# Kernel optimization log

Hardware: AMD Instinct MI355X
Metric: run time of the kernel (lower is better)

The kernel has to match this reference:

```python
import jax, jax.numpy as jnp
import numpy as np

HEADS, DIM_HEAD, DIM = 12, 64, 768
H = W = 32
N = H * W
B = 4


def _ln(x, g, b, eps=1e-5):
    mu = x.mean(-1, keepdims=True)
    var = ((x - mu) ** 2).mean(-1, keepdims=True)
    return (x - mu) / jnp.sqrt(var + eps) * g + b


def _get_epipolar(k, src_c2w, target_c2w, h=H, w=W):
    # Faithful port of Epipolar_Attention.get_epipolar, without the (hw*hw,3) repeat
    # materialization (uses broadcasting for the pairwise cross product instead).
    b = k.shape[0]
    Wf = h * 16.0 / 9.0
    k = k.astype(jnp.float32)
    k = k.at[:, 0, :].multiply(Wf).at[:, 1, :].multiply(float(h))
    k = k.at[:, 0, 2].set(h / 2.0).at[:, 1, 2].set(h / 2.0)
    ii, jj = jnp.meshgrid(jnp.arange(h), jnp.arange(w), indexing='ij')
    # after the torch column swap: (col, row, 1)
    coords = jnp.stack([jj.ravel(), ii.ravel(), jnp.ones(h * w, jnp.int32)], axis=1).astype(jnp.float32)  # [hw,3]
    k3 = k[:, :3, :3]
    src_r, src_t = src_c2w[:, :3, :3].astype(jnp.float32), src_c2w[:, :3, 3].astype(jnp.float32)
    tgt_r, tgt_t = target_c2w[:, :3, :3].astype(jnp.float32), target_c2w[:, :3, 3].astype(jnp.float32)
    tgt_rinv = jnp.linalg.inv(tgt_r)
    fx, fy = k3[:, 0, 0][:, None], k3[:, 1, 1][:, None]
    cx, cy = k3[:, 0, 2][:, None], k3[:, 1, 2][:, None]
    nc = jnp.stack([(coords[None, :, 0] - cx) / fx,
                    (coords[None, :, 1] - cy) / fy,
                    jnp.broadcast_to(coords[None, :, 2], (b, h * w))], axis=-1)  # [b,hw,3]
    p3w = jnp.einsum('bij,bnj->bni', src_r, nc) + src_t[:, None]
    p2 = jnp.einsum('bij,bnj->bni', tgt_rinv, p3w) - tgt_t[:, None]  # target_w2c_t = -target_c2w_t
    pij_un = jnp.einsum('bij,bnj->bni', k3, p2)                      # [b,hw,3]
    pij = pij_un / (pij_un[..., -1:] + 1e-6)
    o2 = jnp.einsum('bij,bj->bi', tgt_rinv, src_t) - tgt_t           # origin projected
    oij = jnp.einsum('bij,bj->bi', k3, o2)
    oij = oij / oij[..., -1:]
    oi_to_pi = pij - oij[:, None]                # [b,hw,3]
    oi_to_coord = coords[None] - oij[:, None]    # [b,hw,3]
    cr = jnp.cross(oi_to_pi[:, :, None, :], oi_to_coord[:, None, :, :])  # [b,hw,hw,3]
    area = jnp.sqrt((cr * cr).sum(-1))
    vlen = jnp.sqrt((oi_to_pi * oi_to_pi).sum(-1))[:, :, None]
    dist = area / vlen
    dw = 1.0 - jax.nn.sigmoid(50.0 * (dist - 0.5))
    row_max = dw.max(-1, keepdims=True)
    return jnp.where(row_max < 0.5, 1.0, dw)     # rows with max<0.5 are set to all-ones


def setup_inputs():
    key = jax.random.key(0)
    ks = jax.random.split(key, 16)
    s = 0.02
    x = jax.random.normal(ks[0], (B, N, DIM), jnp.float32)
    src_encode = jax.random.normal(ks[1], (B, N, DIM), jnp.float32)
    intrinsic = (jnp.zeros((B, 4, 4), jnp.float32)
                 .at[:, 0, 0].set(1.0).at[:, 1, 1].set(1.0)
                 .at[:, 0, 2].set(0.5).at[:, 1, 2].set(0.5)
                 .at[:, 2, 2].set(1.0).at[:, 3, 3].set(1.0))
    R = jnp.eye(3, dtype=jnp.float32) + 0.1 * jax.random.normal(ks[2], (2, B, 3, 3), jnp.float32)
    t = 0.5 * jax.random.normal(ks[3], (2, B, 3), jnp.float32)
    c2w = (jnp.zeros((2, B, 4, 4), jnp.float32)
           .at[:, :, :3, :3].set(R).at[:, :, :3, 3].set(t).at[:, :, 3, 3].set(1.0))
    hd = HEADS * DIM_HEAD
    w_ = lambda k_, shp: s * jax.random.normal(k_, shp, jnp.float32)
    return dict(
        x=x, src_encode=src_encode, intrinsic=intrinsic, c2w=c2w,
        lnq_g=jnp.ones(DIM), lnq_b=jnp.zeros(DIM), Wq=w_(ks[4], (DIM, hd)), bq=jnp.zeros(hd),
        lnk_g=jnp.ones(DIM), lnk_b=jnp.zeros(DIM), Wk=w_(ks[5], (DIM, hd)), bk=jnp.zeros(hd),
        lnv_g=jnp.ones(DIM), lnv_b=jnp.zeros(DIM), Wv=w_(ks[6], (DIM, hd)), bv=jnp.zeros(hd),
        Wp=w_(ks[7], (hd, DIM)), bp=jnp.zeros(DIM),
        pre_g=jnp.ones(DIM), pre_b=jnp.zeros(DIM),
        W1=w_(ks[8], (DIM, 2 * DIM)), b1=jnp.zeros(2 * DIM),
        W2=w_(ks[9], (2 * DIM, DIM)), b2=jnp.zeros(DIM),
        post_g=jnp.ones(DIM), post_b=jnp.zeros(DIM))


def reference(x, src_encode, intrinsic, c2w, lnq_g, lnq_b, Wq, bq, lnk_g, lnk_b, Wk, bk,
              lnv_g, lnv_b, Wv, bv, Wp, bp, pre_g, pre_b, W1, b1, W2, b2, post_g, post_b):
    b, n, _ = x.shape
    scale = DIM_HEAD ** -0.5
    split = lambda t_: t_.reshape(b, n, HEADS, DIM_HEAD).transpose(0, 2, 1, 3)  # [b,m,n,d]
    q = split(_ln(x, lnq_g, lnq_b) @ Wq + bq)
    k = split(_ln(src_encode, lnk_g, lnk_b) @ Wk + bk)
    v = split(_ln(src_encode, lnv_g, lnv_b) @ Wv + bv)
    scores = scale * jnp.einsum('bmqd,bmkd->bmqk', q, k)
    e1 = _get_epipolar(intrinsic, c2w[1], c2w[0])                    # do_epipolar
    e2 = jnp.swapaxes(_get_epipolar(intrinsic, c2w[0], c2w[1]), 1, 2)  # bidirectional (transposed)
    wmap = e1 * e2                                                   # [b,n,n], shared across heads
    att = jax.nn.softmax(scores * wmap[:, None], axis=-1)
    a = jnp.einsum('bmqk,bmkd->bmqd', att, v).transpose(0, 2, 1, 3).reshape(b, n, HEADS * DIM_HEAD)
    z = _ln(a @ Wp + bp, pre_g, pre_b)
    z = z + (jax.nn.gelu(z @ W1 + b1, approximate=False) @ W2 + b2)  # torch nn.GELU = exact erf
    z = _ln(z, post_g, post_b)
    wm_full = jnp.broadcast_to(wmap[:, None], (b, HEADS, n, n)).reshape(b * HEADS, n, n)
    return z, wm_full
```

## Files before the change

### kernel.cpp

```cpp
#include <hip/hip_runtime.h>
#include <hip/hip_bf16.h>

typedef unsigned short u16;
typedef __attribute__((ext_vector_type(4))) unsigned short u16x4;
typedef __attribute__((ext_vector_type(8))) unsigned short u16x8;
typedef __attribute__((ext_vector_type(8))) short s16x8;
typedef __attribute__((ext_vector_type(4))) float f32x4;

#define HEADS 12
#define NSEQ 1024
#define DIMM 768
#define DHEAD 64

__device__ __forceinline__ float b2f(u16 h) {
  union { unsigned u; float f; } v; v.u = ((unsigned)h) << 16; return v.f;
}
__device__ __forceinline__ u16 f2b(float f) {
  union { float f; unsigned u; } v; v.f = f;
  unsigned r = v.u + 0x7fffu + ((v.u >> 16) & 1u);
  return (u16)(r >> 16);
}
__device__ __forceinline__ void gl_lds16(const u16* g, u16* l) {
  __builtin_amdgcn_global_load_lds(
      (const __attribute__((address_space(1))) void*)g,
      (__attribute__((address_space(3))) void*)l, 16, 0, 0);
}

template<bool GELU, bool RESID, bool VTOUT>
__device__ __forceinline__ void gemm64(
    const u16* __restrict__ A, const u16* __restrict__ BT,
    const float* __restrict__ bias, const u16* __restrict__ resid,
    const float* __restrict__ rg, const float* __restrict__ rb,
    u16* __restrict__ C, int K, int lda, int ldb, int ldc,
    int m0, int n0, u16* As, u16* Bs, u16* __restrict__ vt)
{
  const int tid = threadIdx.x;
  const int lane = tid & 63;
  const int wv = tid >> 6;
  const int wm0 = (wv >> 1) * 32;
  const int wn0 = (wv & 1) * 32;
  const int l15 = lane & 15;
  const int quad = lane >> 4;
  const int srow = wv * 8 + (lane >> 3);
  const int schunk = lane & 7;
  const int scol = (schunk ^ (srow & 7)) * 8;

  f32x4 acc[2][2];
  #pragma unroll
  for (int i = 0; i < 2; ++i)
    #pragma unroll
    for (int j = 0; j < 2; ++j)
      acc[i][j] = {0.f, 0.f, 0.f, 0.f};

  const u16* Ab = A + (long)(m0 + srow) * lda + scol;
  const u16* Bb = BT + (long)(n0 + srow) * ldb + scol;

  auto issue = [&](int buf, int kk) {
    #pragma unroll
    for (int s = 0; s < 2; ++s) {
      gl_lds16(Ab + kk + (long)s * 32 * lda, As + buf * 4096 + s * 2048 + wv * 512);
      gl_lds16(Bb + kk + (long)s * 32 * ldb, Bs + buf * 4096 + s * 2048 + wv * 512);
    }
  };

  const int NK = K >> 6;
  issue(0, 0);
  issue(1, 64);

  int cur = 0;
  for (int i = 0; i < NK; ++i) {
    if (i + 1 < NK) asm volatile("s_waitcnt vmcnt(4)" ::: "memory");
    else            asm volatile("s_waitcnt vmcnt(0)" ::: "memory");
    __builtin_amdgcn_s_barrier();
    __builtin_amdgcn_sched_barrier(0);
    if (i + 2 < NK) {
      int nb = cur + 2; if (nb >= 3) nb -= 3;
      issue(nb, (i + 2) * 64);
    }
    const u16* Ac = As + cur * 4096;
    const u16* Bc = Bs + cur * 4096;
    #pragma unroll
    for (int kk = 0; kk < 2; ++kk) {
      s16x8 af[2], bfr[2];
      #pragma unroll
      for (int i2 = 0; i2 < 2; ++i2)
        af[i2] = *(const s16x8*)&Ac[(wm0 + i2 * 16 + l15) * 64 +
                                    (((kk * 4 + quad) ^ (l15 & 7)) * 8)];
      #pragma unroll
      for (int j = 0; j < 2; ++j)
        bfr[j] = *(const s16x8*)&Bc[(wn0 + j * 16 + l15) * 64 +
                                    (((kk * 4 + quad) ^ (l15 & 7)) * 8)];
      #pragma unroll
      for (int i2 = 0; i2 < 2; ++i2)
        #pragma unroll
        for (int j = 0; j < 2; ++j)
          acc[i2][j] = __builtin_amdgcn_mfma_f32_16x16x32_bf16(af[i2], bfr[j], acc[i2][j], 0, 0, 0);
    }
    ++cur; if (cur == 3) cur = 0;
  }

  if (VTOUT) {
    __syncthreads();
    u16* shp = As;
    const int b = m0 >> 10;
    const int nloc = m0 & 1023;
    const int fb0 = n0 - 768;
    #pragma unroll
    for (int j = 0; j < 2; ++j) {
      const float bvv = bias[n0 + wn0 + j * 16 + l15];
      #pragma unroll
      for (int i = 0; i < 2; ++i)
        #pragma unroll
        for (int v = 0; v < 4; ++v)
          shp[(wm0 + i * 16 + quad * 4 + v) * 72 + (wn0 + j * 16 + l15)] =
              f2b(acc[i][j][v] + bvv);
    }
    __syncthreads();
    const int f = tid >> 2;
    const int nb = (tid & 3) * 16;
    u16x8 o0, o1;
    #pragma unroll
    for (int nn = 0; nn < 8; ++nn) {
      o0[nn] = shp[(nb + nn) * 72 + f];
      o1[nn] = shp[(nb + 8 + nn) * 72 + f];
    }
    u16* dst = vt + ((long)(b * 768 + fb0 + f)) * NSEQ + nloc + nb;
    *(u16x8*)&dst[0] = o0;
    *(u16x8*)&dst[8] = o1;
    return;
  }

  #pragma unroll
  for (int i = 0; i < 2; ++i)
    #pragma unroll
    for (int j = 0; j < 2; ++j) {
      const int col = n0 + wn0 + j * 16 + l15;
      const float bvv = bias[col];
      #pragma unroll
      for (int v = 0; v < 4; ++v) {
        const int row = m0 + wm0 + i * 16 + quad * 4 + v;
        float val = acc[i][j][v] + bvv;
        if (GELU) val = 0.5f * val * (1.0f + erff(val * 0.70710678118654752440f));
        if (RESID) val += b2f(resid[(long)row * ldc + col]) * rg[col] + rb[col];
        C[(long)row * ldc + col] = f2b(val);
      }
    }
}

template<bool GELU, bool RESID>
__global__ __launch_bounds__(256)
void gemm_one(const u16* __restrict__ A, const u16* __restrict__ BT,
              const float* __restrict__ bias, const u16* __restrict__ resid,
              const float* __restrict__ rg, const float* __restrict__ rb,
              u16* __restrict__ C, int K, int lda, int ldb, int ldc)
{
  __shared__ u16 As[12288], Bs[12288];
  const int total = gridDim.x * gridDim.y;
  const int fid = blockIdx.y * gridDim.x + blockIdx.x;
  const int swz = (fid & 7) * (total >> 3) + (fid >> 3);
  const int x = swz & 63;
  const int y = swz >> 6;
  gemm64<GELU, RESID, false>(A, BT, bias, resid, rg, rb, C, K, lda, ldb, ldc,
                             x * 64, y * 64, As, Bs, nullptr);
}

__device__ __forceinline__ float dwval(f32x4 U, float ox, float oy, float oz, int m)
{
  const float cx = (float)(m & 31) - ox;
  const float cy = (float)(m >> 5) - oy;
  const float cz = 1.0f - oz;
  const float crx = U.y * cz - U.z * cy;
  const float cry = U.z * cx - U.x * cz;
  const float crz = U.x * cy - U.y * cx;
  const float area = sqrtf(crx * crx + cry * cry + crz * crz);
  const float dist = area / U.w;
  const float t = 50.0f * (dist - 0.5f);
  return 1.0f - 1.0f / (1.0f + __expf(-t));
}

#define PREP_T0 13824
#define PREP_T1 14016
#define PREP_T2 22208
#define PREP_T3 30400

__global__ __launch_bounds__(256)
void prep2(const float* w0, const float* w1, const float* w2,
           const float* w3, const float* w4, const float* w5,
           const float* gq, const float* gk, const float* gv, const float* gp,
           u16* d0, u16* d12, u16* d3, u16* d4, u16* d5,
           const float* bq, const float* bk, const float* bv, const float* b1,
           const float* lnqb, const float* lnkb, const float* lnvb, const float* preb,
           float* obq, float* obkv, float* ob1,
           const float* intr, const float* c2w,
           float* u4, float* oijb, float* flags,
           const float* nx, const float* nsrc, u16* onx, u16* onsrc)
{
  const int bid = blockIdx.x;
  const int tid = threadIdx.x;

  if (bid < PREP_T0) {
    __shared__ u16 t[32][36];
    const int z = bid / 2304;
    const int rem = bid - z * 2304;
    const int bx = rem % 48, by = rem / 48;
    const float* src; const float* g; u16* dst; int R, C; float sc = 1.0f;
    switch (z) {
      case 0: src = w0; g = gq; dst = d0;  R = 768;  C = 768;  sc = 0.125f; break;
      case 1: src = w1; g = gk; dst = d12; R = 768;  C = 768;  break;
      case 2: src = w2; g = gv; dst = d12 + 768 * 768; R = 768; C = 768; break;
      case 3: src = w3; g = nullptr; dst = d3; R = 768;  C = 768;  break;
      case 4: src = w4; g = gp; dst = d4; R = 768;  C = 1536; break;
      default: src = w5; g = nullptr; dst = d5; R = 1536; C = 768; break;
    }
    const int c0 = bx * 32;
    const int r0 = by * 32;
    if (c0 >= C || r0 >= R) return;
    const int i = tid >> 3;
    const int j4 = (tid & 7) * 4;
    const float rs = (g ? g[r0 + i] : 1.0f) * sc;
    #pragma unroll
    for (int jj = 0; jj < 4; ++jj)
      t[i][j4 + jj] = f2b(src[(long)(r0 + i) * C + c0 + j4 + jj] * rs);
    __syncthreads();
    u16x4 ov;
    #pragma unroll
    for (int jj = 0; jj < 4; ++jj) ov[jj] = t[j4 + jj][i];
    *(u16x4*)&dst[(long)(c0 + i) * R + r0 + j4] = ov;
    return;
  }

  if (bid < PREP_T1) {
    __shared__ float red[8][32];
    const int idx = bid - PREP_T0;
    const int y = idx / 48;
    const int bx = idx % 48;
    const float* W; const float* bln; const float* bw; float* out;
    int C; float sc = 1.0f;
    switch (y) {
      case 0: W = w0; bln = lnqb; bw = bq; out = obq;        C = 768;  sc = 0.125f; break;
      case 1: W = w1; bln = lnkb; bw = bk; out = obkv;       C = 768;  break;
      case 2: W = w2; bln = lnvb; bw = bv; out = obkv + 768; C = 768;  break;
      default: W = w4; bln = preb; bw = b1; out = ob1;       C = 1536; break;
    }
    const int c0 = bx * 32;
    if (c0 >= C) return;
    const int cl = tid & 31;
    const int rg = tid >> 5;
    const int c = c0 + cl;
    float s = 0.f;
    for (int r = rg * 96; r < rg * 96 + 96; ++r)
      s += bln[r] * W[(long)r * C + c];
    red[rg][cl] = s;
    __syncthreads();
    if (rg == 0) {
      float tot = bw[c];
      #pragma unroll
      for (int k = 0; k < 8; ++k) tot += red[k][cl];
      out[c] = tot * sc;
    }
    return;
  }

  if (bid < PREP_T2) {
    __shared__ float S[40];
    __shared__ float redf[8];
    const int rowid = bid - PREP_T1;
    const int db = rowid >> 10;
    const int n = rowid & 1023;
    const int d = db >> 2, b = db & 3;
    if (tid == 0) {
      const int sidx = (d == 0) ? 1 : 0;
      const int tidx = 1 - sidx;
      float k3[9], sr[9], st[3], tr[9], tt[3];
      const float Wf = 32.0f * 16.0f / 9.0f;
      for (int j = 0; j < 3; ++j) {
        k3[j]     = intr[(b * 4 + 0) * 4 + j] * Wf;
        k3[3 + j] = intr[(b * 4 + 1) * 4 + j] * 32.0f;
        k3[6 + j] = intr[(b * 4 + 2) * 4 + j];
      }
      k3[2] = 16.0f; k3[5] = 16.0f;
      for (int i = 0; i < 3; ++i) {
        for (int j = 0; j < 3; ++j) {
          sr[i * 3 + j] = c2w[((sidx * 4 + b) * 4 + i) * 4 + j];
          tr[i * 3 + j] = c2w[((tidx * 4 + b) * 4 + i) * 4 + j];
        }
        st[i] = c2w[((sidx * 4 + b) * 4 + i) * 4 + 3];
        tt[i] = c2w[((tidx * 4 + b) * 4 + i) * 4 + 3];
      }
      double a = tr[0], bb_ = tr[1], c = tr[2];
      double dd2 = tr[3], e = tr[4], f = tr[5];
      double g2 = tr[6], h2 = tr[7], i2 = tr[8];
      double det = a * (e * i2 - f * h2) - bb_ * (dd2 * i2 - f * g2) + c * (dd2 * h2 - e * g2);
      double inv[9] = {
        (e * i2 - f * h2), (c * h2 - bb_ * i2), (bb_ * f - c * e),
        (f * g2 - dd2 * i2), (a * i2 - c * g2), (c * dd2 - a * f),
        (dd2 * h2 - e * g2), (bb_ * g2 - a * h2), (a * e - bb_ * dd2)
      };
      float tri[9];
      for (int t2 = 0; t2 < 9; ++t2) tri[t2] = (float)(inv[t2] / det);
      float o2[3], oij[3];
      for (int i3 = 0; i3 < 3; ++i3)
        o2[i3] = tri[i3 * 3] * st[0] + tri[i3 * 3 + 1] * st[1] + tri[i3 * 3 + 2] * st[2] - tt[i3];
      for (int i3 = 0; i3 < 3; ++i3)
        oij[i3] = k3[i3 * 3] * o2[0] + k3[i3 * 3 + 1] * o2[1] + k3[i3 * 3 + 2] * o2[2];
      const float ozf = oij[2];
      oij[0] = oij[0] / ozf; oij[1] = oij[1] / ozf; oij[2] = ozf / ozf;
      if (n == 0) {
        oijb[db * 4 + 0] = oij[0]; oijb[db * 4 + 1] = oij[1];
        oijb[db * 4 + 2] = oij[2]; oijb[db * 4 + 3] = 0.f;
      }
      const float ncx = ((float)(n & 31) - k3[2]) / k3[0];
      const float ncy = ((float)(n >> 5) - k3[5]) / k3[4];
      const float p0 = sr[0] * ncx + sr[1] * ncy + sr[2] + st[0];
      const float p1 = sr[3] * ncx + sr[4] * ncy + sr[5] + st[1];
      const float p2 = sr[6] * ncx + sr[7] * ncy + sr[8] + st[2];
      const float q0 = tri[0] * p0 + tri[1] * p1 + tri[2] * p2 - tt[0];
      const float q1 = tri[3] * p0 + tri[4] * p1 + tri[5] * p2 - tt[1];
      const float q2 = tri[6] * p0 + tri[7] * p1 + tri[8] * p2 - tt[2];
      const float ww0 = k3[0] * q0 + k3[1] * q1 + k3[2] * q2;
      const float ww1 = k3[3] * q0 + k3[4] * q1 + k3[5] * q2;
      const float ww2 = k3[6] * q0 + k3[7] * q1 + k3[8] * q2;
      const float pz = ww2 + 1e-6f;
      const float ux = ww0 / pz - oij[0];
      const float uy = ww1 / pz - oij[1];
      const float uz = ww2 / pz - oij[2];
      const float vlen = sqrtf(ux * ux + uy * uy + uz * uz);
      f32x4 uo = {ux, uy, uz, vlen};
      *(f32x4*)&u4[(long)rowid * 4] = uo;
      S[33] = oij[0]; S[34] = oij[1]; S[35] = oij[2];
      S[36] = ux; S[37] = uy; S[38] = uz; S[39] = vlen;
    }
    __syncthreads();
    const f32x4 U = {S[36], S[37], S[38], S[39]};
    const float ox = S[33], oy = S[34], oz = S[35];
    float mx = -1e30f;
    #pragma unroll
    for (int i = 0; i < 4; ++i)
      mx = fmaxf(mx, dwval(U, ox, oy, oz, tid + i * 256));
    #pragma unroll
    for (int off = 32; off; off >>= 1) mx = fmaxf(mx, __shfl_down(mx, off));
    const int lane = tid & 63, wid = tid >> 6;
    if (!lane) redf[wid] = mx;
    __syncthreads();
    if (!tid) {
      const float m4 = fmaxf(fmaxf(redf[0], redf[1]), fmaxf(redf[2], redf[3]));
      flags[rowid] = (m4 < 0.5f) ? 1.0f : 0.0f;
    }
    return;
  }

  {
    __shared__ float s1[8], s2[8];
    const int r = bid - PREP_T2;
    const float* p = ((r < 4096) ? nx : nsrc) + (long)(r & 4095) * DIMM;
    u16* o = ((r < 4096) ? onx : onsrc) + (long)(r & 4095) * DIMM;
    float v0 = p[tid], v1 = p[tid + 256], v2 = p[tid + 512];
    float s = v0 + v1 + v2;
    #pragma unroll
    for (int off = 32; off; off >>= 1) s += __shfl_down(s, off);
    const int lane = tid & 63, wid = tid >> 6;
    if (!lane) s1[wid] = s;
    __syncthreads();
    if (!tid) s1[4] = s1[0] + s1[1] + s1[2] + s1[3];
    __syncthreads();
    const float mu = s1[4] / 768.0f;
    float d0 = v0 - mu, d1 = v1 - mu, d2 = v2 - mu;
    float sq = d0 * d0 + d1 * d1 + d2 * d2;
    #pragma unroll
    for (int off = 32; off; off >>= 1) sq += __shfl_down(sq, off);
    if (!lane) s2[wid] = sq;
    __syncthreads();
    if (!tid) s2[4] = s2[0] + s2[1] + s2[2] + s2[3];
    __syncthreads();
    const float rstd = 1.0f / sqrtf(s2[4] / 768.0f + 1e-5f);
    o[tid]       = f2b(d0 * rstd);
    o[tid + 256] = f2b(d1 * rstd);
    o[tid + 512] = f2b(d2 * rstd);
  }
}

__global__ __launch_bounds__(256)
void stageB(const u16* __restrict__ nx, const u16* __restrict__ ns,
            const u16* __restrict__ qT, const u16* __restrict__ kvT,
            const float* __restrict__ bqf, const float* __restrict__ bkvf,
            u16* __restrict__ qb, u16* __restrict__ kvb, u16* __restrict__ vT,
            const float* __restrict__ u4, const float* __restrict__ oijb,
            const float* __restrict__ flags,
            u16* __restrict__ wm2, float* __restrict__ wm_full)
{
  __shared__ __align__(16) u16 sh[24576];
  const int bid = blockIdx.x;
  const int tid = threadIdx.x;

  if (bid < 2304) {
    u16* As = sh;
    u16* Bs = sh + 12288;
    const int swz = (bid & 7) * 288 + (bid >> 3);
    const int z = swz / 768;
    const int idx = swz - z * 768;
    const int x = idx & 63;
    const int y = idx >> 6;
    if (z == 0)
      gemm64<false, false, false>(nx, qT, bqf, nullptr, nullptr, nullptr, qb,
                                  768, 768, 768, 768,
                                  x * 64, y * 64, As, Bs, nullptr);
    else if (z == 1)
      gemm64<false, false, false>(ns, kvT, bkvf, nullptr, nullptr, nullptr, kvb,
                                  768, 768, 768, 1536,
                                  x * 64, y * 64, As, Bs, nullptr);
    else
      gemm64<false, false, true>(ns, kvT, bkvf, nullptr, nullptr, nullptr, nullptr,
                                 768, 768, 768, 1536,
                                 x * 64, 768 + y * 64, As, Bs, vT);
    return;
  }

  const int id = bid - 2304;
  const int qx = id & 31;
  const int ky = (id >> 5) & 31;
  const int b = id >> 10;
  const int q0 = qx * 32;
  const int k0 = ky * 32;
  const int i = tid >> 3;
  const int j4 = (tid & 7) * 4;

  f32x4* U2s = (f32x4*)sh;
  float* f2s = (float*)(sh + 256);
  float* f1s = (float*)(sh + 320);
  if (tid < 32) {
    U2s[tid] = *(const f32x4*)&u4[((long)(4 + b) * 1024 + k0 + tid) * 4];
    f2s[tid] = flags[(4 + b) * 1024 + k0 + tid];
    f1s[tid] = flags[b * 1024 + q0 + tid];
  }
  __syncthreads();

  const int q = q0 + i;
  const f32x4 U1 = *(const f32x4*)&u4[((long)b * 1024 + q) * 4];
  const float o1x = oijb[b * 4 + 0], o1y = oijb[b * 4 + 1], o1z = oijb[b * 4 + 2];
  const float o2x = oijb[(4 + b) * 4 + 0], o2y = oijb[(4 + b) * 4 + 1], o2z = oijb[(4 + b) * 4 + 2];
  const bool fl1 = f1s[i] > 0.5f;

  const int Q = q >> 6;
  const int qr = q & 63;
  const int wv2 = qr >> 4, qd = (qr >> 2) & 3, v2 = qr & 3;
  const int kt = (k0 + j4) >> 6;
  u16* w2base = wm2 + ((((long)b * 16 + Q) * 16 + kt) * 256) * 16;

  f32x4 wf;
  #pragma unroll
  for (int jj = 0; jj < 4; ++jj) {
    const int k = k0 + j4 + jj;
    const float e1 = fl1 ? 1.0f : dwval(U1, o1x, o1y, o1z, k);
    const float e2 = (f2s[j4 + jj] > 0.5f) ? 1.0f : dwval(U2s[j4 + jj], o2x, o2y, o2z, q);
    const float w = e1 * e2;
    wf[jj] = w;
    const int kc = k & 63;
    const int j2 = kc >> 4, l2 = kc & 15;
    const int ftid = wv2 * 64 + qd * 16 + l2;
    w2base[ftid * 16 + j2 * 4 + v2] = f2b(w);
  }
  #pragma unroll
  for (int h = 0; h < HEADS; ++h)
    *(f32x4*)&wm_full[((long)(b * HEADS + h) * 1024 + q0 + i) * 1024 + k0 + j4] = wf;
}

__global__ __launch_bounds__(256, 3)
void fattn(const u16* __restrict__ qb, const u16* __restrict__ kvb,
           const u16* __restrict__ vT, const u16* __restrict__ wm2,
           u16* __restrict__ outA)
{
  __shared__ u16 Qs[2 * 64 * 32];
  __shared__ u16 Ks[2][2 * 64 * 32];
  __shared__ u16 Vs[2][2 * 64 * 32];
  __shared__ u16 Ps[64][72];

  const int fid = blockIdx.x;
  const int swz = (fid & 7) * 96 + (fid >> 3);
  const int b = swz / 192;
  const int r = swz - b * 192;
  const int x = r / 12;
  const int h = r - x * 12;
  const int bh = b * HEADS + h;
  const int q0 = x * 64;
  const int tid = threadIdx.x;
  const int lane = tid & 63;
  const int wv = tid >> 6;
  const int l15 = lane & 15;
  const int quad = lane >> 4;
  const int srow = lane >> 2;
  const int sscol = ((lane & 3) ^ ((lane >> 3) & 3)) * 8;
  const int rch = (quad ^ ((l15 >> 1) & 3)) * 8;

  const u16* Qg = qb + ((long)b * NSEQ + q0) * DIMM + h * DHEAD;
  const u16* Kg = kvb + (long)b * NSEQ * 1536 + h * DHEAD;
  const u16* Vg = vT + (long)bh * DHEAD * NSEQ;
  const u16* W2 = wm2 + ((((long)b * 16 + x) * 16) * 256) * 16;

  #pragma unroll
  for (int h2 = 0; h2 < 2; ++h2) {
    gl_lds16(Qg + (long)(wv * 16 + srow) * DIMM + h2 * 32 + sscol,
             Qs + (h2 * 64 + wv * 16) * 32);
    gl_lds16(Kg + (long)(wv * 16 + srow) * 1536 + h2 * 32 + sscol,
             Ks[0] + (h2 * 64 + wv * 16) * 32);
    gl_lds16(Vg + (long)(wv * 16 + srow) * NSEQ + h2 * 32 + sscol,
             Vs[0] + (h2 * 64 + wv * 16) * 32);
  }

  f32x4 Sacc[4], Oacc[4];
  float mrow[4], lrow[4];
  #pragma unroll
  for (int j = 0; j < 4; ++j) {
    Oacc[j] = {0.f, 0.f, 0.f, 0.f};
    mrow[j] = -3.0e38f;
    lrow[j] = 0.f;
  }
  s16x8 qf[2];

  int cur = 0;
  for (int kt = 0; kt < 16; ++kt) {
    __syncthreads();
    if (kt < 15) {
      const int nxt = cur ^ 1;
      #pragma unroll
      for (int h2 = 0; h2 < 2; ++h2) {
        gl_lds16(Kg + (long)((kt + 1) * 64 + wv * 16 + srow) * 1536 + h2 * 32 + sscol,
                 Ks[nxt] + (h2 * 64 + wv * 16) * 32);
        gl_lds16(Vg + (long)(wv * 16 + srow) * NSEQ + (kt + 1) * 64 + h2 * 32 + sscol,
                 Vs[nxt] + (h2 * 64 + wv * 16) * 32);
      }
    }

    if (kt == 0) {
      qf[0] = *(const s16x8*)&Qs[(0 * 64 + wv * 16 + l15) * 32 + rch];
      qf[1] = *(const s16x8*)&Qs[(1 * 64 + wv * 16 + l15) * 32 + rch];
    }

    const u16x8 wa = *(const u16x8*)&W2[((long)kt * 256 + tid) * 16];
    const u16x8 wb = *(const u16x8*)&W2[((long)kt * 256 + tid) * 16 + 8];
    float wr[4][4];
    #pragma unroll
    for (int v = 0; v < 4; ++v) {
      wr[0][v] = b2f(wa[v]);
      wr[1][v] = b2f(wa[4 + v]);
      wr[2][v] = b2f(wb[v]);
      wr[3][v] = b2f(wb[4 + v]);
    }

    #pragma unroll
    for (int j = 0; j < 4; ++j) Sacc[j] = {0.f, 0.f, 0.f, 0.f};
    #pragma unroll
    for (int j = 0; j < 4; ++j)
      #pragma unroll
      for (int h2 = 0; h2 < 2; ++h2) {
        s16x8 kf = *(const s16x8*)&Ks[cur][(h2 * 64 + j * 16 + l15) * 32 + rch];
        Sacc[j] = __builtin_amdgcn_mfma_f32_16x16x32_bf16(qf[h2], kf, Sacc[j], 0, 0, 0);
      }

    #pragma unroll
    for (int j = 0; j < 4; ++j)
      #pragma unroll
      for (int v = 0; v < 4; ++v)
        Sacc[j][v] *= wr[j][v];
    #pragma unroll
    for (int v = 0; v < 4; ++v) {
      float tm = fmaxf(fmaxf(Sacc[0][v], Sacc[1][v]), fmaxf(Sacc[2][v], Sacc[3][v]));
      tm = fmaxf(tm, __shfl_xor(tm, 1));
      tm = fmaxf(tm, __shfl_xor(tm, 2));
      tm = fmaxf(tm, __shfl_xor(tm, 4));
      tm = fmaxf(tm, __shfl_xor(tm, 8));
      const float mnew = fmaxf(mrow[v], tm);
      const float al = __expf(mrow[v] - mnew);
      float rs = 0.f;
      #pragma unroll
      for (int j = 0; j < 4; ++j) {
        const float e = __expf(Sacc[j][v] - mnew);
        Sacc[j][v] = e;
        rs += e;
      }
      rs += __shfl_xor(rs, 1);
      rs += __shfl_xor(rs, 2);
      rs += __shfl_xor(rs, 4);
      rs += __shfl_xor(rs, 8);
      lrow[v] = lrow[v] * al + rs;
      mrow[v] = mnew;
      #pragma unroll
      for (int jn = 0; jn < 4; ++jn) Oacc[jn][v] *= al;
    }
    #pragma unroll
    for (int j = 0; j < 4; ++j)
      #pragma unroll
      for (int v = 0; v < 4; ++v)
        Ps[wv * 16 + quad * 4 + v][j * 16 + l15] = f2b(Sacc[j][v]);

    #pragma unroll
    for (int h2 = 0; h2 < 2; ++h2) {
      s16x8 af = *(const s16x8*)&Ps[wv * 16 + l15][h2 * 32 + quad * 8];
      #pragma unroll
      for (int jn = 0; jn < 4; ++jn) {
        s16x8 vf = *(const s16x8*)&Vs[cur][(h2 * 64 + jn * 16 + l15) * 32 + rch];
        Oacc[jn] = __builtin_amdgcn_mfma_f32_16x16x32_bf16(af, vf, Oacc[jn], 0, 0, 0);
      }
    }
    cur ^= 1;
  }

  #pragma unroll
  for (int v = 0; v < 4; ++v) {
    const int row = q0 + wv * 16 + quad * 4 + v;
    const float inv = 1.0f / lrow[v];
    #pragma unroll
    for (int jn = 0; jn < 4; ++jn)
      outA[((long)(b * NSEQ + row)) * DIMM + h * DHEAD + jn * 16 + l15] =
          f2b(Oacc[jn][v] * inv);
  }
}

__global__ __launch_bounds__(256)
void norm_k(const u16* __restrict__ in, u16* __restrict__ out)
{
  const long base = (long)blockIdx.x * DIMM;
  const int tid = threadIdx.x;
  __shared__ float s1[8], s2[8];
  const u16* p = in + base;
  float v0 = b2f(p[tid]), v1 = b2f(p[tid + 256]), v2 = b2f(p[tid + 512]);
  float s = v0 + v1 + v2;
  #pragma unroll
  for (int off = 32; off; off >>= 1) s += __shfl_down(s, off);
  const int lane = tid & 63, wid = tid >> 6;
  if (!lane) s1[wid] = s;
  __syncthreads();
  if (!tid) s1[4] = s1[0] + s1[1] + s1[2] + s1[3];
  __syncthreads();
  const float mu = s1[4] / 768.0f;
  float d0 = v0 - mu, d1 = v1 - mu, d2 = v2 - mu;
  float sq = d0 * d0 + d1 * d1 + d2 * d2;
  #pragma unroll
  for (int off = 32; off; off >>= 1) sq += __shfl_down(sq, off);
  if (!lane) s2[wid] = sq;
  __syncthreads();
  if (!tid) s2[4] = s2[0] + s2[1] + s2[2] + s2[3];
  __syncthreads();
  const float rstd = 1.0f / sqrtf(s2[4] / 768.0f + 1e-5f);
  u16* o = out + base;
  o[tid]       = f2b(d0 * rstd);
  o[tid + 256] = f2b(d1 * rstd);
  o[tid + 512] = f2b(d2 * rstd);
}

__global__ __launch_bounds__(256)
void ln_final(const u16* __restrict__ in, const float* __restrict__ g,
              const float* __restrict__ bb, float* __restrict__ out)
{
  const long base = (long)blockIdx.x * DIMM;
  const int tid = threadIdx.x;
  __shared__ float s1[8], s2[8];
  const u16* p = in + base;
  float v0 = b2f(p[tid]), v1 = b2f(p[tid + 256]), v2 = b2f(p[tid + 512]);
  float s = v0 + v1 + v2;
  #pragma unroll
  for (int off = 32; off; off >>= 1) s += __shfl_down(s, off);
  const int lane = tid & 63, wid = tid >> 6;
  if (!lane) s1[wid] = s;
  __syncthreads();
  if (!tid) s1[4] = s1[0] + s1[1] + s1[2] + s1[3];
  __syncthreads();
  const float mu = s1[4] / 768.0f;
  float d0 = v0 - mu, d1 = v1 - mu, d2 = v2 - mu;
  float sq = d0 * d0 + d1 * d1 + d2 * d2;
  #pragma unroll
  for (int off = 32; off; off >>= 1) sq += __shfl_down(sq, off);
  if (!lane) s2[wid] = sq;
  __syncthreads();
  if (!tid) s2[4] = s2[0] + s2[1] + s2[2] + s2[3];
  __syncthreads();
  const float rstd = 1.0f / sqrtf(s2[4] / 768.0f + 1e-5f);
  float* o = out + base;
  o[tid]       = d0 * rstd * g[tid]       + bb[tid];
  o[tid + 256] = d1 * rstd * g[tid + 256] + bb[tid + 256];
  o[tid + 512] = d2 * rstd * g[tid + 512] + bb[tid + 512];
}

extern "C" void kernel_launch(void* const* d_in, const int* in_sizes, int n_in,
                              void* d_out, int out_size, void* d_ws, size_t ws_size,
                              hipStream_t stream)
{
  (void)in_sizes; (void)n_in; (void)out_size; (void)ws_size;
  const float* x     = (const float*)d_in[0];
  const float* src   = (const float*)d_in[1];
  const float* intr  = (const float*)d_in[2];
  const float* c2w   = (const float*)d_in[3];
  const float* lnq_g = (const float*)d_in[4];
  const float* lnq_b = (const float*)d_in[5];
  const float* Wq    = (const float*)d_in[6];
  const float* bq    = (const float*)d_in[7];
  const float* lnk_g = (const float*)d_in[8];
  const float* lnk_b = (const float*)d_in[9];
  const float* Wk    = (const float*)d_in[10];
  const float* bk    = (const float*)d_in[11];
  const float* lnv_g = (const float*)d_in[12];
  const float* lnv_b = (const float*)d_in[13];
  const float* Wv    = (const float*)d_in[14];
  const float* bv    = (const float*)d_in[15];
  const float* Wp    = (const float*)d_in[16];
  const float* bp    = (const float*)d_in[17];
  const float* pre_g = (const float*)d_in[18];
  const float* pre_b = (const float*)d_in[19];
  const float* W1    = (const float*)d_in[20];
  const float* b1    = (const float*)d_in[21];
  const float* W2    = (const float*)d_in[22];
  const float* b2    = (const float*)d_in[23];
  const float* post_g= (const float*)d_in[24];
  const float* post_b= (const float*)d_in[25];

  char* ws = (char*)d_ws;
  size_t off = 0;
  auto alloc = [&](size_t bytes) -> char* {
    char* p = ws + off;
    off = (off + bytes + 255) & ~(size_t)255;
    return p;
  };
  const size_t SEQD = (size_t)4096 * 768 * 2;

  u16* WqT  = (u16*)alloc(768 * 768 * 2);
  u16* WkvT = (u16*)alloc((size_t)1536 * 768 * 2);
  u16* WpT  = (u16*)alloc(768 * 768 * 2);
  u16* W1T  = (u16*)alloc(768 * 1536 * 2);
  u16* W2T  = (u16*)alloc(1536 * 768 * 2);
  float* bqf  = (float*)alloc(768 * 4);
  float* bkvf = (float*)alloc(1536 * 4);
  float* b1f  = (float*)alloc(1536 * 4);
  char* pool = alloc(6 * SEQD);
  float* u4   = (float*)alloc(8 * 1024 * 4 * 4);
  float* oijb = (float*)alloc(8 * 4 * 4);
  u16* wm2b   = (u16*)alloc((size_t)4 * 1024 * 1024 * 2);
  float* flagb = (float*)alloc(8 * 1024 * 4);

  u16* S0 = (u16*)pool;
  u16* S1 = (u16*)(pool + SEQD);
  u16* S2 = (u16*)(pool + 2 * SEQD);
  u16* S3 = (u16*)(pool + 3 * SEQD);
  u16* S5 = (u16*)(pool + 5 * SEQD);

  float* out_z  = (float*)d_out;
  float* out_wm = (float*)d_out + (size_t)4 * 1024 * 768;

  prep2<<<PREP_T3, 256, 0, stream>>>(
      Wq, Wk, Wv, Wp, W1, W2, lnq_g, lnk_g, lnv_g, pre_g,
      WqT, WkvT, WpT, W1T, W2T,
      bq, bk, bv, b1, lnq_b, lnk_b, lnv_b, pre_b,
      bqf, bkvf, b1f,
      intr, c2w, u4, oijb, flagb,
      x, src, S0, S1);

  stageB<<<6400, 256, 0, stream>>>(
      S0, S1, WqT, WkvT, bqf, bkvf, S2, S3, S5,
      u4, oijb, flagb, wm2b, out_wm);

  fattn<<<768, 256, 0, stream>>>(S2, S3, S5, wm2b, S0);

  gemm_one<false, false><<<dim3(64, 12), 256, 0, stream>>>(
      S0, WpT, bp, nullptr, nullptr, nullptr, S1, 768, 768, 768, 768);

  norm_k<<<4096, 256, 0, stream>>>(S1, S2);

  gemm_one<true, false><<<dim3(64, 24), 256, 0, stream>>>(
      S2, W1T, b1f, nullptr, nullptr, nullptr, S3, 768, 768, 768, 1536);

  gemm_one<false, true><<<dim3(64, 12), 256, 0, stream>>>(
      S3, W2T, b2, S2, pre_g, pre_b, S5, 1536, 1536, 1536, 768);

  ln_final<<<4096, 256, 0, stream>>>(S5, post_g, post_b, out_z);
}
```

Baseline: 467.1 us.

## Enlarge GEMM tiles to 128x128 with double buffering and nontemporal weight-map stores

Every GEMM now uses 128x128 block tiles: each wave computes a 64x64 sub-tile with a 4x4 MFMA accumulator array, and a 2-stage LDS buffer replaces the 3-stage ring. Grid sizes and the stageB block split are updated to match, and the V-transpose epilogue is done in two 64-row passes. The aim is more operand reuse and fewer global loads per FLOP. In exchange there are far fewer blocks (192-576 per GEMM on a 256-CU part), more registers per wave, and a shallower prefetch pipeline. The large wm_full broadcast writes also become nontemporal stores to reduce cache pollution.

```diff
diff --git a/kernel.cpp b/kernel.cpp
--- a/kernel.cpp
+++ b/kernel.cpp
@@ -27,7 +27,7 @@
 }
 
 template<bool GELU, bool RESID, bool VTOUT>
-__device__ __forceinline__ void gemm64(
+__device__ __forceinline__ void gemm128(
     const u16* __restrict__ A, const u16* __restrict__ BT,
     const float* __restrict__ bias, const u16* __restrict__ resid,
     const float* __restrict__ rg, const float* __restrict__ rb,
@@ -37,19 +37,18 @@
   const int tid = threadIdx.x;
   const int lane = tid & 63;
   const int wv = tid >> 6;
-  const int wm0 = (wv >> 1) * 32;
-  const int wn0 = (wv & 1) * 32;
+  const int wm0 = (wv >> 1) * 64;
+  const int wn0 = (wv & 1) * 64;
   const int l15 = lane & 15;
   const int quad = lane >> 4;
   const int srow = wv * 8 + (lane >> 3);
-  const int schunk = lane & 7;
-  const int scol = (schunk ^ (srow & 7)) * 8;
-
-  f32x4 acc[2][2];
-  #pragma unroll
-  for (int i = 0; i < 2; ++i)
-    #pragma unroll
-    for (int j = 0; j < 2; ++j)
+  const int scol = ((lane & 7) ^ (lane >> 3)) * 8;
+
+  f32x4 acc[4][4];
+  #pragma unroll
+  for (int i = 0; i < 4; ++i)
+    #pragma unroll
+    for (int j = 0; j < 4; ++j)
       acc[i][j] = {0.f, 0.f, 0.f, 0.f};
 
   const u16* Ab = A + (long)(m0 + srow) * lda + scol;
@@ -57,83 +56,85 @@
 
   auto issue = [&](int buf, int kk) {
     #pragma unroll
-    for (int s = 0; s < 2; ++s) {
-      gl_lds16(Ab + kk + (long)s * 32 * lda, As + buf * 4096 + s * 2048 + wv * 512);
-      gl_lds16(Bb + kk + (long)s * 32 * ldb, Bs + buf * 4096 + s * 2048 + wv * 512);
+    for (int s = 0; s < 4; ++s) {
+      gl_lds16(Ab + kk + (long)s * 32 * lda, As + buf * 8192 + s * 2048 + wv * 512);
+      gl_lds16(Bb + kk + (long)s * 32 * ldb, Bs + buf * 8192 + s * 2048 + wv * 512);
     }
   };
 
   const int NK = K >> 6;
   issue(0, 0);
-  issue(1, 64);
 
   int cur = 0;
   for (int i = 0; i < NK; ++i) {
-    if (i + 1 < NK) asm volatile("s_waitcnt vmcnt(4)" ::: "memory");
-    else            asm volatile("s_waitcnt vmcnt(0)" ::: "memory");
+    asm volatile("s_waitcnt vmcnt(0)" ::: "memory");
     __builtin_amdgcn_s_barrier();
     __builtin_amdgcn_sched_barrier(0);
-    if (i + 2 < NK) {
-      int nb = cur + 2; if (nb >= 3) nb -= 3;
-      issue(nb, (i + 2) * 64);
-    }
-    const u16* Ac = As + cur * 4096;
-    const u16* Bc = Bs + cur * 4096;
+    if (i + 1 < NK) issue(cur ^ 1, (i + 1) * 64);
+    const u16* Ac = As + cur * 8192;
+    const u16* Bc = Bs + cur * 8192;
     #pragma unroll
     for (int kk = 0; kk < 2; ++kk) {
-      s16x8 af[2], bfr[2];
-      #pragma unroll
-      for (int i2 = 0; i2 < 2; ++i2)
+      s16x8 af[4], bfr[4];
+      #pragma unroll
+      for (int i2 = 0; i2 < 4; ++i2)
         af[i2] = *(const s16x8*)&Ac[(wm0 + i2 * 16 + l15) * 64 +
                                     (((kk * 4 + quad) ^ (l15 & 7)) * 8)];
       #pragma unroll
-      for (int j = 0; j < 2; ++j)
+      for (int j = 0; j < 4; ++j)
         bfr[j] = *(const s16x8*)&Bc[(wn0 + j * 16 + l15) * 64 +
                                     (((kk * 4 + quad) ^ (l15 & 7)) * 8)];
       #pragma unroll
-      for (int i2 = 0; i2 < 2; ++i2)
+      for (int i2 = 0; i2 < 4; ++i2)
         #pragma unroll
-        for (int j = 0; j < 2; ++j)
+        for (int j = 0; j < 4; ++j)
           acc[i2][j] = __builtin_amdgcn_mfma_f32_16x16x32_bf16(af[i2], bfr[j], acc[i2][j], 0, 0, 0);
     }
-    ++cur; if (cur == 3) cur = 0;
+    cur ^= 1;
   }
 
   if (VTOUT) {
     __syncthreads();
     u16* shp = As;
     const int b = m0 >> 10;
-    const int nloc = m0 & 1023;
+    const int nloc0 = m0 & 1023;
     const int fb0 = n0 - 768;
     #pragma unroll
-    for (int j = 0; j < 2; ++j) {
-      const float bvv = bias[n0 + wn0 + j * 16 + l15];
-      #pragma unroll
-      for (int i = 0; i < 2; ++i)
+    for (int p = 0; p < 2; ++p) {
+      if ((wv >> 1) == p) {
         #pragma unroll
-        for (int v = 0; v < 4; ++v)
-          shp[(wm0 + i * 16 + quad * 4 + v) * 72 + (wn0 + j * 16 + l15)] =
-              f2b(acc[i][j][v] + bvv);
-    }
-    __syncthreads();
-    const int f = tid >> 2;
-    const int nb = (tid & 3) * 16;
-    u16x8 o0, o1;
-    #pragma unroll
-    for (int nn = 0; nn < 8; ++nn) {
-      o0[nn] = shp[(nb + nn) * 72 + f];
-      o1[nn] = shp[(nb + 8 + nn) * 72 + f];
-    }
-    u16* dst = vt + ((long)(b * 768 + fb0 + f)) * NSEQ + nloc + nb;
-    *(u16x8*)&dst[0] = o0;
-    *(u16x8*)&dst[8] = o1;
+        for (int j = 0; j < 4; ++j) {
+          const float bvv = bias[n0 + wn0 + j * 16 + l15];
+          #pragma unroll
+          for (int i2 = 0; i2 < 4; ++i2)
+            #pragma unroll
+            for (int v = 0; v < 4; ++v)
+              shp[(i2 * 16 + quad * 4 + v) * 136 + (wn0 + j * 16 + l15)] =
+                  f2b(acc[i2][j][v] + bvv);
+        }
+      }
+      __syncthreads();
+      {
+        const int f = tid >> 1;
+        const int nb = (tid & 1) * 32;
+        u16* dst = vt + ((long)(b * 768 + fb0 + f)) * NSEQ + nloc0 + p * 64 + nb;
+        #pragma unroll
+        for (int c4 = 0; c4 < 4; ++c4) {
+          u16x8 o;
+          #pragma unroll
+          for (int nn = 0; nn < 8; ++nn) o[nn] = shp[(nb + c4 * 8 + nn) * 136 + f];
+          *(u16x8*)&dst[c4 * 8] = o;
+        }
+      }
+      __syncthreads();
+    }
     return;
   }
 
   #pragma unroll
-  for (int i = 0; i < 2; ++i)
-    #pragma unroll
-    for (int j = 0; j < 2; ++j) {
+  for (int i = 0; i < 4; ++i)
+    #pragma unroll
+    for (int j = 0; j < 4; ++j) {
       const int col = n0 + wn0 + j * 16 + l15;
       const float bvv = bias[col];
       #pragma unroll
@@ -154,14 +155,14 @@
               const float* __restrict__ rg, const float* __restrict__ rb,
               u16* __restrict__ C, int K, int lda, int ldb, int ldc)
 {
-  __shared__ u16 As[12288], Bs[12288];
+  __shared__ u16 As[16384], Bs[16384];
   const int total = gridDim.x * gridDim.y;
   const int fid = blockIdx.y * gridDim.x + blockIdx.x;
   const int swz = (fid & 7) * (total >> 3) + (fid >> 3);
-  const int x = swz & 63;
-  const int y = swz >> 6;
-  gemm64<GELU, RESID, false>(A, BT, bias, resid, rg, rb, C, K, lda, ldb, ldc,
-                             x * 64, y * 64, As, Bs, nullptr);
+  const int x = swz & 31;
+  const int y = swz >> 5;
+  gemm128<GELU, RESID, false>(A, BT, bias, resid, rg, rb, C, K, lda, ldb, ldc,
+                              x * 128, y * 128, As, Bs, nullptr);
 }
 
 __device__ __forceinline__ float dwval(f32x4 U, float ox, float oy, float oz, int m)
@@ -388,34 +389,34 @@
             const float* __restrict__ flags,
             u16* __restrict__ wm2, float* __restrict__ wm_full)
 {
-  __shared__ __align__(16) u16 sh[24576];
+  __shared__ __align__(16) u16 sh[32768];
   const int bid = blockIdx.x;
   const int tid = threadIdx.x;
 
-  if (bid < 2304) {
+  if (bid < 576) {
     u16* As = sh;
-    u16* Bs = sh + 12288;
-    const int swz = (bid & 7) * 288 + (bid >> 3);
-    const int z = swz / 768;
-    const int idx = swz - z * 768;
-    const int x = idx & 63;
-    const int y = idx >> 6;
+    u16* Bs = sh + 16384;
+    const int swz = (bid & 7) * 72 + (bid >> 3);
+    const int z = swz / 192;
+    const int idx = swz - z * 192;
+    const int x = idx & 31;
+    const int y = idx >> 5;
     if (z == 0)
-      gemm64<false, false, false>(nx, qT, bqf, nullptr, nullptr, nullptr, qb,
-                                  768, 768, 768, 768,
-                                  x * 64, y * 64, As, Bs, nullptr);
+      gemm128<false, false, false>(nx, qT, bqf, nullptr, nullptr, nullptr, qb,
+                                   768, 768, 768, 768,
+                                   x * 128, y * 128, As, Bs, nullptr);
     else if (z == 1)
-      gemm64<false, false, false>(ns, kvT, bkvf, nullptr, nullptr, nullptr, kvb,
+      gemm128<false, false, false>(ns, kvT, bkvf, nullptr, nullptr, nullptr, kvb,
+                                   768, 768, 768, 1536,
+                                   x * 128, y * 128, As, Bs, nullptr);
+    else
+      gemm128<false, false, true>(ns, kvT, bkvf, nullptr, nullptr, nullptr, nullptr,
                                   768, 768, 768, 1536,
-                                  x * 64, y * 64, As, Bs, nullptr);
-    else
-      gemm64<false, false, true>(ns, kvT, bkvf, nullptr, nullptr, nullptr, nullptr,
-                                 768, 768, 768, 1536,
-                                 x * 64, 768 + y * 64, As, Bs, vT);
+                                  x * 128, 768 + y * 128, As, Bs, vT);
     return;
   }
 
-  const int id = bid - 2304;
+  const int id = bid - 576;
   const int qx = id & 31;
   const int ky = (id >> 5) & 31;
   const int b = id >> 10;
@@ -461,7 +462,8 @@
   }
   #pragma unroll
   for (int h = 0; h < HEADS; ++h)
-    *(f32x4*)&wm_full[((long)(b * HEADS + h) * 1024 + q0 + i) * 1024 + k0 + j4] = wf;
+    __builtin_nontemporal_store(
+        wf, (f32x4*)&wm_full[((long)(b * HEADS + h) * 1024 + q0 + i) * 1024 + k0 + j4]);
 }
 
 __global__ __launch_bounds__(256, 3)
@@ -752,21 +754,21 @@
       intr, c2w, u4, oijb, flagb,
       x, src, S0, S1);
 
-  stageB<<<6400, 256, 0, stream>>>(
+  stageB<<<4672, 256, 0, stream>>>(
       S0, S1, WqT, WkvT, bqf, bkvf, S2, S3, S5,
       u4, oijb, flagb, wm2b, out_wm);
 
   fattn<<<768, 256, 0, stream>>>(S2, S3, S5, wm2b, S0);
 
-  gemm_one<false, false><<<dim3(64, 12), 256, 0, stream>>>(
+  gemm_one<false, false><<<dim3(32, 6), 256, 0, stream>>>(
       S0, WpT, bp, nullptr, nullptr, nullptr, S1, 768, 768, 768, 768);
 
   norm_k<<<4096, 256, 0, stream>>>(S1, S2);
 
-  gemm_one<true, false><<<dim3(64, 24), 256, 0, stream>>>(
+  gemm_one<true, false><<<dim3(32, 12), 256, 0, stream>>>(
       S2, W1T, b1f, nullptr, nullptr, nullptr, S3, 768, 768, 768, 1536);
 
-  gemm_one<false, true><<<dim3(64, 12), 256, 0, stream>>>(
+  gemm_one<false, true><<<dim3(32, 6), 256, 0, stream>>>(
       S3, W2T, b2, S2, pre_g, pre_b, S5, 1536, 1536, 1536, 768);
 
   ln_final<<<4096, 256, 0, stream>>>(S5, post_g, post_b, out_z);
```

Result: no change. 462.8 us (-0.9%).
